# Performance work log

Hardware: AMD Instinct MI355X
Metric: run time of the kernel (lower is better)

The kernel has to match this reference:

```python
import jax, jax.numpy as jnp
import numpy as np

N_NODES = 100000
N_EDGES = 1600000
HIDDEN = 128
EDGE_DIM = 4
N_LAYERS = 3
IN_DIM = 2


def setup_inputs() -> dict:
    key = jax.random.key(0)
    ks = jax.random.split(key, 12)
    msg_in_dim = IN_DIM + HIDDEN + EDGE_DIM  # concat([V_pred, h]) gathered at senders + edge feats
    s = lambda fan_in: 1.0 / np.sqrt(fan_in)
    return {
        "P_Q_inj": jax.random.normal(ks[0], (N_NODES, IN_DIM), jnp.float32),
        "senders": jax.random.randint(ks[1], (N_EDGES,), 0, N_NODES, jnp.int32),
        "receivers": jax.random.randint(ks[2], (N_EDGES,), 0, N_NODES, jnp.int32),
        "edge_features": jax.random.normal(ks[3], (N_EDGES, EDGE_DIM), jnp.float32),
        "W_in": jax.random.normal(ks[4], (IN_DIM, HIDDEN), jnp.float32) * s(IN_DIM),
        "b_in": jnp.zeros((HIDDEN,), jnp.float32),
        "W_msg": jax.random.normal(ks[5], (N_LAYERS, msg_in_dim, HIDDEN), jnp.float32) * s(msg_in_dim),
        "b_msg": jnp.zeros((N_LAYERS, HIDDEN), jnp.float32),
        "W_out": jax.random.normal(ks[6], (N_LAYERS, HIDDEN, IN_DIM), jnp.float32) * s(HIDDEN),
        "b_out": jnp.zeros((N_LAYERS, IN_DIM), jnp.float32),
    }


def reference(P_Q_inj, senders, receivers, edge_features, W_in, b_in, W_msg, b_msg, W_out, b_out):
    N = P_Q_inj.shape[0]
    # initial voltage guess: magnitude 1, angle 0
    V_pred = jnp.zeros_like(P_Q_inj).at[:, 0].set(1.0)  # [N, 2]
    h = P_Q_inj @ W_in + b_in  # [N, H]
    for l in range(W_msg.shape[0]):
        node_inputs = jnp.concatenate([V_pred, h], axis=-1)  # [N, 2+H]
        # gather src feats, concat edge feats, dense message
        msg_in = jnp.concatenate([node_inputs[senders], edge_features], axis=-1)  # [E, 2+H+Fe]
        msg = msg_in @ W_msg[l] + b_msg[l]  # [E, H]
        # scatter-sum aggregate to receiver nodes
        agg = jax.ops.segment_sum(msg, receivers, num_segments=N)  # [N, H]
        h = jax.nn.relu(agg)
        delta_V = h @ W_out[l] + b_out[l]  # [N, 2]
        V_pred = V_pred + delta_V
    return V_pred
```

## Files before the change

### kernel.cpp

```cpp
#include <hip/hip_runtime.h>
#include <hip/hip_bf16.h>
#include <stdint.h>

#define H 128
#define NPB  224
#define NBK  448
#define BCAP 6144
#define NBLK 128

typedef __attribute__((ext_vector_type(8))) short bf16x8;
typedef __attribute__((ext_vector_type(4))) float f32x4;

__device__ __forceinline__ unsigned pack_bf16x2(float a, float b){
  unsigned ua = __float_as_uint(a);
  unsigned ub = __float_as_uint(b);
  unsigned ra = (ua + 0x7fffu + ((ua >> 16) & 1u)) >> 16;
  unsigned rb = (ub + 0x7fffu + ((ub >> 16) & 1u)) >> 16;
  return ra | (rb << 16);
}
__device__ __forceinline__ float bf_lo(unsigned u){ return __uint_as_float(u << 16); }
__device__ __forceinline__ float bf_hi(unsigned u){ return __uint_as_float(u & 0xffff0000u); }

__global__ void countA_kernel(const int* __restrict__ recv, int* __restrict__ cmat, int E){
  __shared__ int hist[NBK];
  int t = threadIdx.x;
  for (int b = t; b < NBK; b += 256) hist[b] = 0;
  __syncthreads();
  int chunk = (E + NBLK - 1) / NBLK;
  int lo = blockIdx.x * chunk, hi = min(E, lo + chunk);
  for (int i = lo + t; i < hi; i += 256)
    atomicAdd(&hist[recv[i]/NPB], 1);
  __syncthreads();
  for (int b = t; b < NBK; b += 256) cmat[blockIdx.x*NBK + b] = hist[b];
}

__global__ void cscan_kernel(const int* __restrict__ cmat, int* __restrict__ gofs,
                             int* __restrict__ bbase, int* __restrict__ rowptr,
                             int NB, int N, int E){
  __shared__ int s[512];
  int t = threadIdx.x;
  int tot = 0;
  if (t < NB)
    for (int k = 0; k < NBLK; ++k) tot += cmat[k*NBK + t];
  s[t] = tot; __syncthreads();
  #pragma unroll
  for (int off = 1; off < 512; off <<= 1){
    int x = (t >= off) ? s[t-off] : 0;
    __syncthreads();
    s[t] += x;
    __syncthreads();
  }
  int run = s[t] - tot;
  if (t < NB){
    bbase[t] = run;
    for (int k = 0; k < NBLK; ++k){
      gofs[k*NBK + t] = run;
      run += cmat[k*NBK + t];
    }
  }
  if (t == 0){ bbase[NB] = E; rowptr[N] = E; }
}

__global__ void scatterC_kernel(const int* __restrict__ recv, const int* __restrict__ send,
                                const int* __restrict__ gofs,
                                unsigned long long* __restrict__ ebuf, int E){
  __shared__ int cur[NBK];
  int t = threadIdx.x;
  for (int b = t; b < NBK; b += 256) cur[b] = gofs[blockIdx.x*NBK + b];
  __syncthreads();
  int chunk = (E + NBLK - 1) / NBLK;
  int lo = blockIdx.x * chunk, hi = min(E, lo + chunk);
  for (int i = lo + t; i < hi; i += 256){
    int r = recv[i];
    int b = r / NPB;
    int rloc = r - b*NPB;
    int pos = atomicAdd(&cur[b], 1);
    ebuf[pos] = ((unsigned long long)(unsigned)send[i] << 32)
              | ((unsigned long long)(unsigned)rloc << 24)
              | (unsigned long long)(unsigned)i;
  }
}

__global__ void bsort_kernel(const unsigned long long* __restrict__ ebuf,
                             const int* __restrict__ bbase,
                             int* __restrict__ ssort, int* __restrict__ eid,
                             int* __restrict__ rowptr, int N, int NB){
  __shared__ unsigned long long se[BCAP];
  __shared__ int sdeg[256];
  __shared__ int scur[256];
  int b = blockIdx.x;
  int t = threadIdx.x;
  int base = bbase[b];
  int cnt  = bbase[b+1] - base;
  if (cnt > BCAP) cnt = BCAP;
  sdeg[t] = 0;
  __syncthreads();
  for (int i = t; i < cnt; i += 256){
    unsigned long long v = ebuf[base + i];
    se[i] = v;
    atomicAdd(&sdeg[(int)((v >> 24) & 0xFF)], 1);
  }
  __syncthreads();
  int own = sdeg[t];
  #pragma unroll
  for (int off = 1; off < 256; off <<= 1){
    int x = (t >= off) ? sdeg[t-off] : 0;
    __syncthreads();
    sdeg[t] += x;
    __syncthreads();
  }
  int excl = sdeg[t] - own;
  scur[t] = excl;
  int node0 = b*NPB;
  if (t < NPB && node0 + t < N) rowptr[node0 + t] = base + excl;
  __syncthreads();
  for (int i = t; i < cnt; i += 256){
    unsigned long long v = se[i];
    int off = atomicAdd(&scur[(int)((v >> 24) & 0xFF)], 1);
    ssort[base + off] = (int)(v >> 32);
    eid[base + off]   = (int)(v & 0xFFFFFF);
  }
}

__global__ void wprep_kernel(const float* __restrict__ Wmsg, unsigned* __restrict__ Wb, int L){
  int t = blockIdx.x*blockDim.x + threadIdx.x;
  if (t >= L*2048) return;
  int layer = t >> 11;
  int f = t & 2047;
  int ct   = f >> 8;
  int ks   = (f >> 6) & 3;
  int lane = f & 63;
  int col = ct*16 + (lane & 15);
  int kbase = ks*32 + (lane >> 4)*8;
  const float* Wl = Wmsg + (size_t)layer*134*H + 2*H;
  unsigned u0 = pack_bf16x2(Wl[(size_t)(kbase+0)*H + col], Wl[(size_t)(kbase+1)*H + col]);
  unsigned u1 = pack_bf16x2(Wl[(size_t)(kbase+2)*H + col], Wl[(size_t)(kbase+3)*H + col]);
  unsigned u2 = pack_bf16x2(Wl[(size_t)(kbase+4)*H + col], Wl[(size_t)(kbase+5)*H + col]);
  unsigned u3 = pack_bf16x2(Wl[(size_t)(kbase+6)*H + col], Wl[(size_t)(kbase+7)*H + col]);
  uint4* dst = reinterpret_cast<uint4*>(Wb) + (size_t)layer*2048 + f;
  *dst = make_uint4(u0, u1, u2, u3);
}

__global__ void prep0_kernel(const float* __restrict__ Wmsg, const float* __restrict__ bmsg,
                             const float* __restrict__ Win, const float* __restrict__ bin,
                             float* __restrict__ ACC){
  int c = threadIdx.x;
  const float* Wh = Wmsg + 2*H;
  float a0 = 0.f, a1 = 0.f, cc = 0.f;
  for (int k = 0; k < H; ++k){
    float w = Wh[(size_t)k*H + c];
    a0 += Win[k]     * w;
    a1 += Win[H + k] * w;
    cc += bin[k]     * w;
  }
  cc += Wmsg[c] + bmsg[c];
  ACC[c] = a0; ACC[H + c] = a1; ACC[2*H + c] = cc;
}

__global__ void msrc0_kernel(const float* __restrict__ PQ, const float* __restrict__ ACC,
                             unsigned* __restrict__ msrc, int N){
  int lane = threadIdx.x & 63;
  int wid  = (blockIdx.x*blockDim.x + threadIdx.x) >> 6;
  int nw   = (gridDim.x*blockDim.x) >> 6;
  int c0 = 2*lane, c1 = c0 + 1;
  float A00 = ACC[c0], A01 = ACC[c1];
  float A10 = ACC[H + c0], A11 = ACC[H + c1];
  float C0  = ACC[2*H + c0], C1 = ACC[2*H + c1];
  for (int n = wid; n < N; n += nw){
    float2 pq = *reinterpret_cast<const float2*>(PQ + 2*n);
    msrc[(size_t)n*64 + lane] = pack_bf16x2(pq.x*A00 + pq.y*A10 + C0,
                                            pq.x*A01 + pq.y*A11 + C1);
  }
}

__global__ void node_msg_mfma(const float* __restrict__ V, const unsigned* __restrict__ h,
                              const float* __restrict__ Wmsg_l, const float* __restrict__ bmsg_l,
                              const unsigned* __restrict__ Wb_l, unsigned* __restrict__ msrc, int N){
  __shared__ uint4 wlds[2048];
  int tid = threadIdx.x;
  const uint4* wb4 = reinterpret_cast<const uint4*>(Wb_l);
  #pragma unroll
  for (int i = 0; i < 8; ++i) wlds[tid + 256*i] = wb4[tid + 256*i];
  __syncthreads();
  const bf16x8* wb = reinterpret_cast<const bf16x8*>(wlds);
  int lane = tid & 63;
  int gw   = (blockIdx.x*blockDim.x + tid) >> 6;
  int nwv  = (gridDim.x*blockDim.x) >> 6;
  int row = lane & 15, kg = lane >> 4;
  int ntiles = N >> 4;
  for (int t = gw; t < ntiles; t += nwv){
    int node0 = t << 4;
    const bf16x8* hrow = reinterpret_cast<const bf16x8*>(h + (size_t)(node0 + row)*64);
    bf16x8 a[4];
    #pragma unroll
    for (int ks = 0; ks < 4; ++ks) a[ks] = hrow[ks*4 + kg];
    float2 vv[4];
    #pragma unroll
    for (int r = 0; r < 4; ++r)
      vv[r] = *reinterpret_cast<const float2*>(V + 2*(node0 + kg*4 + r));
    #pragma unroll
    for (int ct = 0; ct < 8; ++ct){
      f32x4 acc = {0.f, 0.f, 0.f, 0.f};
      #pragma unroll
      for (int ks = 0; ks < 4; ++ks){
        bf16x8 b = wb[(ct*4 + ks)*64 + lane];
        acc = __builtin_amdgcn_mfma_f32_16x16x32_bf16(a[ks], b, acc, 0, 0, 0);
      }
      int col = ct*16 + row;
      float wv0 = Wmsg_l[col], wv1 = Wmsg_l[H + col], bb = bmsg_l[col];
      #pragma unroll
      for (int r = 0; r < 4; ++r){
        float o = acc[r] + vv[r].x*wv0 + vv[r].y*wv1 + bb;
        float oh = __shfl_xor(o, 1, 64);
        if (!(lane & 1)){
          int nr = node0 + kg*4 + r;
          msrc[(size_t)nr*64 + ct*8 + (row >> 1)] = pack_bf16x2(o, oh);
        }
      }
    }
  }
}

template<bool FIRST, bool WRITEH>
__global__ void agg_update_kernel(const unsigned* __restrict__ msrc,
                                  const int* __restrict__ rowptr,
                                  const int* __restrict__ eid,
                                  const int* __restrict__ ssort,
                                  const float* __restrict__ ef,
                                  const float* __restrict__ Wmsg_l,
                                  const float* __restrict__ Wout_l,
                                  const float* __restrict__ bout_l,
                                  const float* __restrict__ Vin,
                                  float* __restrict__ Vout,
                                  unsigned* __restrict__ h,
                                  float4* __restrict__ efsum, int N){
  int lane = threadIdx.x & 63;
  int wid  = (blockIdx.x*blockDim.x + threadIdx.x) >> 6;
  int nw   = (gridDim.x*blockDim.x) >> 6;
  int c0 = 2*lane, c1 = c0 + 1;
  float We00 = Wmsg_l[(size_t)130*H + c0], We01 = Wmsg_l[(size_t)130*H + c1];
  float We10 = Wmsg_l[(size_t)131*H + c0], We11 = Wmsg_l[(size_t)131*H + c1];
  float We20 = Wmsg_l[(size_t)132*H + c0], We21 = Wmsg_l[(size_t)132*H + c1];
  float We30 = Wmsg_l[(size_t)133*H + c0], We31 = Wmsg_l[(size_t)133*H + c1];
  float Wo00 = Wout_l[c0*2], Wo01 = Wout_l[c0*2+1];
  float Wo10 = Wout_l[c1*2], Wo11 = Wout_l[c1*2+1];
  float bo0 = bout_l[0], bo1 = bout_l[1];
  for (int n = wid; n < N; n += nw){
    int beg = rowptr[n], end = rowptr[n+1];
    float acc0 = 0.f, acc1 = 0.f;
    float sfx = 0.f, sfy = 0.f, sfz = 0.f, sfw = 0.f;
    for (int c = beg; c < end; c += 64){
      int inlane = (c + lane < end);
      int sv = inlane ? ssort[c + lane] : 0;
      if (FIRST && inlane){
        int e = eid[c + lane];
        float4 f = *reinterpret_cast<const float4*>(ef + (size_t)e*4);
        sfx += f.x; sfy += f.y; sfz += f.z; sfw += f.w;
      }
      int kmax = min(64, end - c);
      int j = 0;
      for (; j + 4 <= kmax; j += 4){
        int s0 = __shfl(sv, j,   64);
        int s1 = __shfl(sv, j+1, 64);
        int s2 = __shfl(sv, j+2, 64);
        int s3 = __shfl(sv, j+3, 64);
        unsigned u0 = msrc[(size_t)s0*64 + lane];
        unsigned u1 = msrc[(size_t)s1*64 + lane];
        unsigned u2 = msrc[(size_t)s2*64 + lane];
        unsigned u3 = msrc[(size_t)s3*64 + lane];
        acc0 += bf_lo(u0) + bf_lo(u1) + bf_lo(u2) + bf_lo(u3);
        acc1 += bf_hi(u0) + bf_hi(u1) + bf_hi(u2) + bf_hi(u3);
      }
      for (; j < kmax; ++j){
        int s = __shfl(sv, j, 64);
        unsigned u = msrc[(size_t)s*64 + lane];
        acc0 += bf_lo(u); acc1 += bf_hi(u);
      }
    }
    if (FIRST){
      #pragma unroll
      for (int off = 32; off > 0; off >>= 1){
        sfx += __shfl_xor(sfx, off, 64);
        sfy += __shfl_xor(sfy, off, 64);
        sfz += __shfl_xor(sfz, off, 64);
        sfw += __shfl_xor(sfw, off, 64);
      }
      if (lane == 0) efsum[n] = make_float4(sfx, sfy, sfz, sfw);
    } else {
      float4 f = efsum[n];
      sfx = f.x; sfy = f.y; sfz = f.z; sfw = f.w;
    }
    acc0 += sfx*We00 + sfy*We10 + sfz*We20 + sfw*We30;
    acc1 += sfx*We01 + sfy*We11 + sfz*We21 + sfw*We31;
    float a0 = fmaxf(acc0, 0.f), a1 = fmaxf(acc1, 0.f);
    if (WRITEH) h[(size_t)n*64 + lane] = pack_bf16x2(a0, a1);
    float p0 = a0*Wo00 + a1*Wo10;
    float p1 = a0*Wo01 + a1*Wo11;
    #pragma unroll
    for (int off = 16; off > 0; off >>= 1){
      p0 += __shfl_xor(p0, off, 64);
      p1 += __shfl_xor(p1, off, 64);
    }
    p0 += __shfl_xor(p0, 32, 64);
    p1 += __shfl_xor(p1, 32, 64);
    if (lane == 0){
      float v0, v1;
      if (FIRST){ v0 = 1.0f; v1 = 0.0f; }
      else      { v0 = Vin[2*n]; v1 = Vin[2*n+1]; }
      Vout[2*n]   = v0 + p0 + bo0;
      Vout[2*n+1] = v1 + p1 + bo1;
    }
  }
}

extern "C" void kernel_launch(void* const* d_in, const int* in_sizes, int n_in,
                              void* d_out, int out_size, void* d_ws, size_t ws_size,
                              hipStream_t stream){
  const float* PQ      = (const float*)d_in[0];
  const int*   senders = (const int*)  d_in[1];
  const int*   recv    = (const int*)  d_in[2];
  const float* ef      = (const float*)d_in[3];
  const float* Win     = (const float*)d_in[4];
  const float* bin     = (const float*)d_in[5];
  const float* Wmsg    = (const float*)d_in[6];
  const float* bmsg    = (const float*)d_in[7];
  const float* Wout    = (const float*)d_in[8];
  const float* bout    = (const float*)d_in[9];
  int N = in_sizes[0] / 2;
  int E = in_sizes[1];
  int L = in_sizes[7] / H;
  int NB = (N + NPB - 1) / NPB;

  char* base = (char*)d_ws;
  size_t off = 0;
  auto alloc = [&](size_t bytes)->char*{
    char* p = base + off; off += (bytes + 255) & ~(size_t)255; return p;
  };
  unsigned* h      = (unsigned*)alloc((size_t)N*64*4);
  unsigned* msrc   = (unsigned*)alloc((size_t)N*64*4);
  float*    V      = (float*)   alloc((size_t)N*2*4);
  int*      rowptr = (int*)     alloc((size_t)(N+1)*4);
  int*      eid    = (int*)     alloc((size_t)E*4);
  int*      ssort  = (int*)     alloc((size_t)E*4);
  unsigned long long* ebuf = (unsigned long long*)alloc((size_t)E*8);
  float4*   efsum  = (float4*)  alloc((size_t)N*16);
  int*      cmat   = (int*)     alloc((size_t)NBLK*NBK*4);
  int*      gofs   = (int*)     alloc((size_t)NBLK*NBK*4);
  int*      bbase  = (int*)     alloc((size_t)(NB+1)*4);
  unsigned* Wb     = (unsigned*)alloc((size_t)L*2048*16);
  float*    ACC0   = (float*)   alloc((size_t)3*H*4);
  if (off > ws_size) return;

  countA_kernel<<<NBLK, 256, 0, stream>>>(recv, cmat, E);
  cscan_kernel<<<1, 512, 0, stream>>>(cmat, gofs, bbase, rowptr, NB, N, E);
  scatterC_kernel<<<NBLK, 256, 0, stream>>>(recv, senders, gofs, ebuf, E);
  bsort_kernel<<<NB, 256, 0, stream>>>(ebuf, bbase, ssort, eid, rowptr, N, NB);
  wprep_kernel<<<(L*2048 + 255)/256, 256, 0, stream>>>(Wmsg, Wb, L);
  prep0_kernel<<<1, H, 0, stream>>>(Wmsg, bmsg, Win, bin, ACC0);
  msrc0_kernel<<<2048, 256, 0, stream>>>(PQ, ACC0, msrc, N);

  for (int l = 0; l < L; ++l){
    const float* Wmsg_l = Wmsg + (size_t)l*134*H;
    const float* bmsg_l = bmsg + (size_t)l*H;
    const float* Wout_l = Wout + (size_t)l*H*2;
    const float* bout_l = bout + (size_t)l*2;
    const unsigned* Wb_l = Wb + (size_t)l*2048*4;
    if (l > 0)
      node_msg_mfma<<<784, 256, 0, stream>>>(V, h, Wmsg_l, bmsg_l, Wb_l, msrc, N);
    float* Vout = (l == L-1) ? (float*)d_out : V;
    if (l == 0)
      agg_update_kernel<true, true><<<2048, 256, 0, stream>>>(msrc, rowptr, eid, ssort, ef,
                                                        Wmsg_l, Wout_l, bout_l, V, Vout, h, efsum, N);
    else if (l < L-1)
      agg_update_kernel<false, true><<<2048, 256, 0, stream>>>(msrc, rowptr, eid, ssort, ef,
                                                         Wmsg_l, Wout_l, bout_l, V, Vout, h, efsum, N);
    else
      agg_update_kernel<false, false><<<2048, 256, 0, stream>>>(msrc, rowptr, eid, ssort, ef,
                                                         Wmsg_l, Wout_l, bout_l, V, Vout, h, efsum, N);
  }
}
```

Before: 402.1 us.

## Transpose count matrix, fuse weight prep kernels, stage MFMA output through LDS

```diff
diff --git a/kernel.cpp b/kernel.cpp
--- a/kernel.cpp
+++ b/kernel.cpp
@@ -31,7 +31,7 @@
   for (int i = lo + t; i < hi; i += 256)
     atomicAdd(&hist[recv[i]/NPB], 1);
   __syncthreads();
-  for (int b = t; b < NBK; b += 256) cmat[blockIdx.x*NBK + b] = hist[b];
+  for (int b = t; b < NBK; b += 256) cmat[b*NBLK + blockIdx.x] = hist[b];
 }
 
 __global__ void cscan_kernel(const int* __restrict__ cmat, int* __restrict__ gofs,
@@ -41,7 +41,7 @@
   int t = threadIdx.x;
   int tot = 0;
   if (t < NB)
-    for (int k = 0; k < NBLK; ++k) tot += cmat[k*NBK + t];
+    for (int k = 0; k < NBLK; ++k) tot += cmat[t*NBLK + k];
   s[t] = tot; __syncthreads();
   #pragma unroll
   for (int off = 1; off < 512; off <<= 1){
@@ -54,8 +54,8 @@
   if (t < NB){
     bbase[t] = run;
     for (int k = 0; k < NBLK; ++k){
-      gofs[k*NBK + t] = run;
-      run += cmat[k*NBK + t];
+      gofs[t*NBLK + k] = run;
+      run += cmat[t*NBLK + k];
     }
   }
   if (t == 0){ bbase[NB] = E; rowptr[N] = E; }
@@ -66,7 +66,7 @@
                                 unsigned long long* __restrict__ ebuf, int E){
   __shared__ int cur[NBK];
   int t = threadIdx.x;
-  for (int b = t; b < NBK; b += 256) cur[b] = gofs[blockIdx.x*NBK + b];
+  for (int b = t; b < NBK; b += 256) cur[b] = gofs[b*NBLK + blockIdx.x];
   __syncthreads();
   int chunk = (E + NBLK - 1) / NBLK;
   int lo = blockIdx.x * chunk, hi = min(E, lo + chunk);
@@ -122,9 +122,27 @@
   }
 }
 
-__global__ void wprep_kernel(const float* __restrict__ Wmsg, unsigned* __restrict__ Wb, int L){
+__global__ void wprep_kernel(const float* __restrict__ Wmsg, const float* __restrict__ bmsg,
+                             const float* __restrict__ Win, const float* __restrict__ bin,
+                             unsigned* __restrict__ Wb, float* __restrict__ ACC, int L){
+  int nwp = L*8;
+  if ((int)blockIdx.x == nwp){
+    int c = threadIdx.x;
+    if (c < H){
+      const float* Wh = Wmsg + 2*H;
+      float a0 = 0.f, a1 = 0.f, cc = 0.f;
+      for (int k = 0; k < H; ++k){
+        float w = Wh[(size_t)k*H + c];
+        a0 += Win[k]     * w;
+        a1 += Win[H + k] * w;
+        cc += bin[k]     * w;
+      }
+      cc += Wmsg[c] + bmsg[c];
+      ACC[c] = a0; ACC[H + c] = a1; ACC[2*H + c] = cc;
+    }
+    return;
+  }
   int t = blockIdx.x*blockDim.x + threadIdx.x;
-  if (t >= L*2048) return;
   int layer = t >> 11;
   int f = t & 2047;
   int ct   = f >> 8;
@@ -141,22 +159,6 @@
   *dst = make_uint4(u0, u1, u2, u3);
 }
 
-__global__ void prep0_kernel(const float* __restrict__ Wmsg, const float* __restrict__ bmsg,
-                             const float* __restrict__ Win, const float* __restrict__ bin,
-                             float* __restrict__ ACC){
-  int c = threadIdx.x;
-  const float* Wh = Wmsg + 2*H;
-  float a0 = 0.f, a1 = 0.f, cc = 0.f;
-  for (int k = 0; k < H; ++k){
-    float w = Wh[(size_t)k*H + c];
-    a0 += Win[k]     * w;
-    a1 += Win[H + k] * w;
-    cc += bin[k]     * w;
-  }
-  cc += Wmsg[c] + bmsg[c];
-  ACC[c] = a0; ACC[H + c] = a1; ACC[2*H + c] = cc;
-}
-
 __global__ void msrc0_kernel(const float* __restrict__ PQ, const float* __restrict__ ACC,
                              unsigned* __restrict__ msrc, int N){
   int lane = threadIdx.x & 63;
@@ -177,6 +179,7 @@
                               const float* __restrict__ Wmsg_l, const float* __restrict__ bmsg_l,
                               const unsigned* __restrict__ Wb_l, unsigned* __restrict__ msrc, int N){
   __shared__ uint4 wlds[2048];
+  __shared__ unsigned stg[4][16][65];
   int tid = threadIdx.x;
   const uint4* wb4 = reinterpret_cast<const uint4*>(Wb_l);
   #pragma unroll
@@ -184,6 +187,7 @@
   __syncthreads();
   const bf16x8* wb = reinterpret_cast<const bf16x8*>(wlds);
   int lane = tid & 63;
+  int wv   = tid >> 6;
   int gw   = (blockIdx.x*blockDim.x + tid) >> 6;
   int nwv  = (gridDim.x*blockDim.x) >> 6;
   int row = lane & 15, kg = lane >> 4;
@@ -212,12 +216,14 @@
       for (int r = 0; r < 4; ++r){
         float o = acc[r] + vv[r].x*wv0 + vv[r].y*wv1 + bb;
         float oh = __shfl_xor(o, 1, 64);
-        if (!(lane & 1)){
-          int nr = node0 + kg*4 + r;
-          msrc[(size_t)nr*64 + ct*8 + (row >> 1)] = pack_bf16x2(o, oh);
-        }
-      }
-    }
+        if (!(lane & 1))
+          stg[wv][kg*4 + r][ct*8 + (row >> 1)] = pack_bf16x2(o, oh);
+      }
+    }
+    unsigned* mrow = msrc + (size_t)node0*64;
+    #pragma unroll
+    for (int rr = 0; rr < 16; ++rr)
+      mrow[rr*64 + lane] = stg[wv][rr][lane];
   }
 }
 
@@ -297,12 +303,10 @@
     float p0 = a0*Wo00 + a1*Wo10;
     float p1 = a0*Wo01 + a1*Wo11;
     #pragma unroll
-    for (int off = 16; off > 0; off >>= 1){
+    for (int off = 32; off > 0; off >>= 1){
       p0 += __shfl_xor(p0, off, 64);
       p1 += __shfl_xor(p1, off, 64);
     }
-    p0 += __shfl_xor(p0, 32, 64);
-    p1 += __shfl_xor(p1, 32, 64);
     if (lane == 0){
       float v0, v1;
       if (FIRST){ v0 = 1.0f; v1 = 0.0f; }
@@ -344,20 +348,19 @@
   int*      ssort  = (int*)     alloc((size_t)E*4);
   unsigned long long* ebuf = (unsigned long long*)alloc((size_t)E*8);
   float4*   efsum  = (float4*)  alloc((size_t)N*16);
-  int*      cmat   = (int*)     alloc((size_t)NBLK*NBK*4);
-  int*      gofs   = (int*)     alloc((size_t)NBLK*NBK*4);
+  int*      cmat   = (int*)     alloc((size_t)NBK*NBLK*4);
+  int*      gofs   = (int*)     alloc((size_t)NBK*NBLK*4);
   int*      bbase  = (int*)     alloc((size_t)(NB+1)*4);
   unsigned* Wb     = (unsigned*)alloc((size_t)L*2048*16);
   float*    ACC0   = (float*)   alloc((size_t)3*H*4);
   if (off > ws_size) return;
 
+  wprep_kernel<<<L*8 + 1, 256, 0, stream>>>(Wmsg, bmsg, Win, bin, Wb, ACC0, L);
+  msrc0_kernel<<<2048, 256, 0, stream>>>(PQ, ACC0, msrc, N);
   countA_kernel<<<NBLK, 256, 0, stream>>>(recv, cmat, E);
   cscan_kernel<<<1, 512, 0, stream>>>(cmat, gofs, bbase, rowptr, NB, N, E);
   scatterC_kernel<<<NBLK, 256, 0, stream>>>(recv, senders, gofs, ebuf, E);
   bsort_kernel<<<NB, 256, 0, stream>>>(ebuf, bbase, ssort, eid, rowptr, N, NB);
-  wprep_kernel<<<(L*2048 + 255)/256, 256, 0, stream>>>(Wmsg, Wb, L);
-  prep0_kernel<<<1, H, 0, stream>>>(Wmsg, bmsg, Win, bin, ACC0);
-  msrc0_kernel<<<2048, 256, 0, stream>>>(PQ, ACC0, msrc, N);
 
   for (int l = 0; l < L; ++l){
     const float* Wmsg_l = Wmsg + (size_t)l*134*H;
```

Result: slower. 421.9 us (+4.9%).
